# Performance work log

Hardware: AMD Instinct MI355X
Metric: run time of the kernel (lower is better)

Reference implementation:

```python
import jax, jax.numpy as jnp
import numpy as np

N_USERS = 100000
N_ITEMS = 50000
N_NODES = N_USERS + N_ITEMS
EMB_DIM = 128
N_LAYERS = 3
NNZ = 2400000
MASK_PROB = 0.2


def setup_inputs() -> dict:
    key = jax.random.key(0)
    ks = jax.random.split(key, 8)
    user_emb = jax.random.normal(ks[0], (N_USERS, EMB_DIM), dtype=jnp.float32) * 0.1
    item_emb = jax.random.normal(ks[1], (N_ITEMS, EMB_DIM), dtype=jnp.float32) * 0.1
    adj_rows = jax.random.randint(ks[2], (NNZ,), 0, N_NODES, dtype=jnp.int32)
    adj_cols = jax.random.randint(ks[3], (NNZ,), 0, N_NODES, dtype=jnp.int32)
    # stand-in for symmetric-normalized adjacency values
    adj_vals = jax.random.uniform(ks[4], (NNZ,), dtype=jnp.float32) * (1.0 / 16.0)
    # deterministic version of mask_embeddings' random binary mask
    mask = (jax.random.uniform(ks[5], (N_USERS, EMB_DIM)) > MASK_PROB).astype(jnp.float32)
    # Dense(emb_dim, relu) params (Glorot-like scale)
    attr_w = jax.random.normal(ks[6], (EMB_DIM, EMB_DIM), dtype=jnp.float32) * (1.0 / np.sqrt(EMB_DIM))
    attr_b = jnp.zeros((EMB_DIM,), dtype=jnp.float32)
    return {"user_emb": user_emb, "item_emb": item_emb, "adj_rows": adj_rows,
            "adj_cols": adj_cols, "adj_vals": adj_vals, "mask": mask,
            "attr_w": attr_w, "attr_b": attr_b}


def _spmm(rows, cols, vals, x):
    # sparse [N,N] @ dense [N,d] via gather + segment_sum
    return jax.ops.segment_sum(vals[:, None] * x[cols], rows, num_segments=N_NODES)


def reference(user_emb, item_emb, adj_rows, adj_cols, adj_vals, mask, attr_w, attr_b):
    alpha = 1.0 / (N_LAYERS + 1)
    all_emb = jnp.concatenate([user_emb, item_emb], axis=0)  # [N, d]
    combined = alpha * all_emb
    for _ in range(N_LAYERS):
        all_emb = _spmm(adj_rows, adj_cols, adj_vals, all_emb)
        combined = combined + alpha * all_emb
    user_final = combined[:N_USERS]
    item_final = combined[N_USERS:]
    masked_user_emb = user_final * mask
    predicted_attributes = jax.nn.relu(masked_user_emb @ attr_w + attr_b)
    return (user_final, item_final, masked_user_emb, predicted_attributes, mask)
```

## Files before the change

### kernel.cpp

```cpp
#include <hip/hip_runtime.h>

#define N_USERS 100000
#define N_ITEMS 50000
#define N_NODES 150000
#define NNZ     2400000
#define ALPHA   0.25f
#define VSCALE  262144.0f
#define VINV    (1.0f / 262144.0f)

static __device__ __forceinline__ int xcd_swz(int orig, int q, int rem) {
    int xcd = orig & 7, idx = orig >> 3;
    return (xcd < rem ? xcd * (q + 1) : rem * (q + 1) + (xcd - rem) * q) + idx;
}

static __device__ __forceinline__ float wave_max64(float m) {
    #pragma unroll
    for (int off = 32; off >= 1; off >>= 1)
        m = fmaxf(m, __shfl_xor(m, off, 64));
    return m;
}

static __device__ __forceinline__ float i8lo(unsigned short w) {
    return (float)(signed char)(w & 0xff);
}
static __device__ __forceinline__ float i8hi(unsigned short w) {
    return (float)(signed char)(w >> 8);
}

__launch_bounds__(256)
__global__ void k_initq(const float2* __restrict__ ue2, const float2* __restrict__ ie2,
                        unsigned short* __restrict__ xq, float* __restrict__ scl) {
    int r = blockIdx.x * 4 + __builtin_amdgcn_readfirstlane(threadIdx.x >> 6);
    if (r >= N_NODES) return;
    int l = threadIdx.x & 63;
    float2 v = (r < N_USERS) ? ue2[r * 64 + l] : ie2[(r - N_USERS) * 64 + l];
    float m = wave_max64(fmaxf(fabsf(v.x), fabsf(v.y)));
    float inv = (m > 0.f) ? 127.0f / m : 0.f;
    int q0 = (int)rintf(v.x * inv), q1 = (int)rintf(v.y * inv);
    xq[r * 64 + l] = (unsigned short)((q0 & 0xff) | ((q1 & 0xff) << 8));
    if (l == 0) scl[r] = m * (1.0f / 127.0f);
}

__global__ void k_histrank(const int* __restrict__ rows, int* __restrict__ cnt,
                           int* __restrict__ rank) {
    int stride = gridDim.x * blockDim.x;
    for (int i = blockIdx.x * blockDim.x + threadIdx.x; i < NNZ; i += stride)
        rank[i] = atomicAdd(&cnt[rows[i]], 1);
}

__global__ void k_scan1(const int* __restrict__ cnt, int* __restrict__ tmp, int* __restrict__ part) {
    __shared__ int sm[1024];
    int g = blockIdx.x * 1024 + threadIdx.x;
    int v = (g < N_NODES) ? cnt[g] : 0;
    sm[threadIdx.x] = v;
    __syncthreads();
    for (int off = 1; off < 1024; off <<= 1) {
        int t = (threadIdx.x >= off) ? sm[threadIdx.x - off] : 0;
        __syncthreads();
        sm[threadIdx.x] += t;
        __syncthreads();
    }
    if (g < N_NODES) tmp[g] = sm[threadIdx.x];
    if (threadIdx.x == 1023) part[blockIdx.x] = sm[1023];
}

__global__ void k_scan2(int* __restrict__ part, int n) {
    __shared__ int sm[256];
    int v = (threadIdx.x < n) ? part[threadIdx.x] : 0;
    sm[threadIdx.x] = v;
    __syncthreads();
    for (int off = 1; off < 256; off <<= 1) {
        int t = (threadIdx.x >= off) ? sm[threadIdx.x - off] : 0;
        __syncthreads();
        sm[threadIdx.x] += t;
        __syncthreads();
    }
    if (threadIdx.x < n) part[threadIdx.x] = sm[threadIdx.x];
}

__global__ void k_scan3(const int* __restrict__ tmp, const int* __restrict__ part, int* __restrict__ rp) {
    int g = blockIdx.x * 1024 + threadIdx.x;
    if (g < N_NODES) {
        int add = blockIdx.x ? part[blockIdx.x - 1] : 0;
        rp[g + 1] = tmp[g] + add;
    }
    if (g == 0) rp[0] = 0;
}

__launch_bounds__(256)
__global__ void k_scatter(const int* __restrict__ rows, const int* __restrict__ cols,
                          const float* __restrict__ vals, const int* __restrict__ rank,
                          const int* __restrict__ rp, unsigned int* __restrict__ ev) {
    int cls = blockIdx.x & 7;
    int base = (blockIdx.x >> 3) * 256 + threadIdx.x;
    for (int i = base; i < NNZ; i += 65536) {
        int r = rows[i];
        if (((r >> 11) & 7) != cls) continue;
        int v14 = (int)(vals[i] * VSCALE + 0.5f);
        v14 = min(v14, 16383);
        unsigned int w = ((unsigned int)cols[i] << 14) | (unsigned int)v14;
        ev[rp[r] + rank[i]] = w;
    }
}

__launch_bounds__(256)
__global__ void k_spmmq(const int* __restrict__ rp, const unsigned int* __restrict__ ev,
                        const unsigned short* __restrict__ xq, const float* __restrict__ sclx,
                        unsigned short* __restrict__ yq, float* __restrict__ scly) {
    int b = xcd_swz(blockIdx.x, 4687, 4);
    int r = b * 4 + __builtin_amdgcn_readfirstlane(threadIdx.x >> 6);
    if (r >= N_NODES) return;
    int l = threadIdx.x & 63;
    float ax = 0.f, ay = 0.f;
    int s = rp[r], e = rp[r + 1];
    int j = s;
    for (; j + 4 <= e; j += 4) {
        unsigned int m0 = ev[j], m1 = ev[j + 1], m2 = ev[j + 2], m3 = ev[j + 3];
        int c0 = __builtin_amdgcn_readfirstlane((int)(m0 >> 14));
        int c1 = __builtin_amdgcn_readfirstlane((int)(m1 >> 14));
        int c2 = __builtin_amdgcn_readfirstlane((int)(m2 >> 14));
        int c3 = __builtin_amdgcn_readfirstlane((int)(m3 >> 14));
        unsigned short w0 = xq[c0 * 64 + l];
        unsigned short w1 = xq[c1 * 64 + l];
        unsigned short w2 = xq[c2 * 64 + l];
        unsigned short w3 = xq[c3 * 64 + l];
        float f0 = (float)(m0 & 16383u) * VINV * sclx[c0];
        float f1 = (float)(m1 & 16383u) * VINV * sclx[c1];
        float f2 = (float)(m2 & 16383u) * VINV * sclx[c2];
        float f3 = (float)(m3 & 16383u) * VINV * sclx[c3];
        ax += f0 * i8lo(w0) + f1 * i8lo(w1) + f2 * i8lo(w2) + f3 * i8lo(w3);
        ay += f0 * i8hi(w0) + f1 * i8hi(w1) + f2 * i8hi(w2) + f3 * i8hi(w3);
    }
    for (; j < e; ++j) {
        unsigned int m = ev[j];
        int c = __builtin_amdgcn_readfirstlane((int)(m >> 14));
        unsigned short w = xq[c * 64 + l];
        float f = (float)(m & 16383u) * VINV * sclx[c];
        ax += f * i8lo(w);
        ay += f * i8hi(w);
    }
    float m = wave_max64(fmaxf(fabsf(ax), fabsf(ay)));
    float inv = (m > 0.f) ? 127.0f / m : 0.f;
    int q0 = (int)rintf(ax * inv), q1 = (int)rintf(ay * inv);
    yq[r * 64 + l] = (unsigned short)((q0 & 0xff) | ((q1 & 0xff) << 8));
    if (l == 0) scly[r] = m * (1.0f / 127.0f);
}

__launch_bounds__(256)
__global__ void k_spmm3q(const int* __restrict__ rp, const unsigned int* __restrict__ ev,
                         const unsigned short* __restrict__ y2q, const float* __restrict__ scl2,
                         const unsigned short* __restrict__ y1q, const float* __restrict__ scl1,
                         const float2* __restrict__ ue2, const float2* __restrict__ ie2,
                         const float2* __restrict__ mask2,
                         float2* __restrict__ comb2, float2* __restrict__ masked2,
                         float2* __restrict__ maskO2) {
    int b = xcd_swz(blockIdx.x, 4687, 4);
    int r = b * 4 + __builtin_amdgcn_readfirstlane(threadIdx.x >> 6);
    if (r >= N_NODES) return;
    int l = threadIdx.x & 63;
    float ax = 0.f, ay = 0.f;
    int s = rp[r], e = rp[r + 1];
    int j = s;
    for (; j + 4 <= e; j += 4) {
        unsigned int m0 = ev[j], m1 = ev[j + 1], m2 = ev[j + 2], m3 = ev[j + 3];
        int c0 = __builtin_amdgcn_readfirstlane((int)(m0 >> 14));
        int c1 = __builtin_amdgcn_readfirstlane((int)(m1 >> 14));
        int c2 = __builtin_amdgcn_readfirstlane((int)(m2 >> 14));
        int c3 = __builtin_amdgcn_readfirstlane((int)(m3 >> 14));
        unsigned short w0 = y2q[c0 * 64 + l];
        unsigned short w1 = y2q[c1 * 64 + l];
        unsigned short w2 = y2q[c2 * 64 + l];
        unsigned short w3 = y2q[c3 * 64 + l];
        float f0 = (float)(m0 & 16383u) * VINV * scl2[c0];
        float f1 = (float)(m1 & 16383u) * VINV * scl2[c1];
        float f2 = (float)(m2 & 16383u) * VINV * scl2[c2];
        float f3 = (float)(m3 & 16383u) * VINV * scl2[c3];
        ax += f0 * i8lo(w0) + f1 * i8lo(w1) + f2 * i8lo(w2) + f3 * i8lo(w3);
        ay += f0 * i8hi(w0) + f1 * i8hi(w1) + f2 * i8hi(w2) + f3 * i8hi(w3);
    }
    for (; j < e; ++j) {
        unsigned int m = ev[j];
        int c = __builtin_amdgcn_readfirstlane((int)(m >> 14));
        unsigned short w = y2q[c * 64 + l];
        float f = (float)(m & 16383u) * VINV * scl2[c];
        ax += f * i8lo(w);
        ay += f * i8hi(w);
    }
    float2 em = (r < N_USERS) ? ue2[r * 64 + l] : ie2[(r - N_USERS) * 64 + l];
    float s1 = scl1[r], s2 = scl2[r];
    unsigned short a1 = y1q[r * 64 + l];
    unsigned short a2 = y2q[r * 64 + l];
    float cx = ALPHA * (em.x + s1 * i8lo(a1) + s2 * i8lo(a2) + ax);
    float cy = ALPHA * (em.y + s1 * i8hi(a1) + s2 * i8hi(a2) + ay);
    comb2[r * 64 + l] = make_float2(cx, cy);
    if (r < N_USERS) {
        float2 m = mask2[r * 64 + l];
        masked2[r * 64 + l] = make_float2(cx * m.x, cy * m.y);
        maskO2[r * 64 + l]  = m;
    }
}

__launch_bounds__(256)
__global__ void k_mm(const float* __restrict__ A, const float* __restrict__ W,
                     const float* __restrict__ b, float* __restrict__ pred) {
    __shared__ float Wl[128 * 128];
    float4* W4s = (float4*)Wl;
    const float4* W4g = (const float4*)W;
    for (int i = threadIdx.x; i < 4096; i += 256) W4s[i] = W4g[i];
    __syncthreads();

    int rowt = threadIdx.x >> 3;
    int colg = threadIdx.x & 7;
    int row  = blockIdx.x * 32 + rowt;
    const float* ar = A + row * 128;

    float4 a0 = make_float4(0, 0, 0, 0), a1 = a0, a2 = a0, a3 = a0;
    for (int k = 0; k < 128; ++k) {
        float av = ar[k];
        float4 w0 = W4s[k * 32 + colg];
        float4 w1 = W4s[k * 32 + colg + 8];
        float4 w2 = W4s[k * 32 + colg + 16];
        float4 w3 = W4s[k * 32 + colg + 24];
        a0.x += av * w0.x; a0.y += av * w0.y; a0.z += av * w0.z; a0.w += av * w0.w;
        a1.x += av * w1.x; a1.y += av * w1.y; a1.z += av * w1.z; a1.w += av * w1.w;
        a2.x += av * w2.x; a2.y += av * w2.y; a2.z += av * w2.z; a2.w += av * w2.w;
        a3.x += av * w3.x; a3.y += av * w3.y; a3.z += av * w3.z; a3.w += av * w3.w;
    }
    const float4* b4 = (const float4*)b;
    float4* out4 = (float4*)pred;
    float4 acc[4] = {a0, a1, a2, a3};
    #pragma unroll
    for (int jj = 0; jj < 4; ++jj) {
        float4 bb = b4[colg + 8 * jj];
        float4 r;
        r.x = fmaxf(acc[jj].x + bb.x, 0.f);
        r.y = fmaxf(acc[jj].y + bb.y, 0.f);
        r.z = fmaxf(acc[jj].z + bb.z, 0.f);
        r.w = fmaxf(acc[jj].w + bb.w, 0.f);
        out4[row * 32 + colg + 8 * jj] = r;
    }
}

extern "C" void kernel_launch(void* const* d_in, const int* in_sizes, int n_in,
                              void* d_out, int out_size, void* d_ws, size_t ws_size,
                              hipStream_t stream) {
    const float* ue     = (const float*)d_in[0];
    const float* ie     = (const float*)d_in[1];
    const int*   arows  = (const int*)d_in[2];
    const int*   acols  = (const int*)d_in[3];
    const float* avals  = (const float*)d_in[4];
    const float* mask   = (const float*)d_in[5];
    const float* attr_w = (const float*)d_in[6];
    const float* attr_b = (const float*)d_in[7];
    float* out = (float*)d_out;

    float* comb   = out;
    float* masked = out + 19200000;
    float* pred   = out + 32000000;
    float* maskO  = out + 44800000;

    char* ws = (char*)d_ws;
    unsigned short* x0q  = (unsigned short*)(ws);
    unsigned short* y1q  = (unsigned short*)(ws + 19200000);
    unsigned short* y2q  = (unsigned short*)(ws + 38400000);
    float*          scl0 = (float*)        (ws + 57600000);
    float*          scl1 = (float*)        (ws + 58200000);
    float*          scl2 = (float*)        (ws + 58800000);
    int*            rank = (int*)          (ws + 59400000);
    unsigned int*   ev   = (unsigned int*) (ws + 69000000);
    int*            cnt  = (int*)          (ws + 78600000);
    int*            rp   = (int*)          (ws + 79200064);
    int*            tmp  = (int*)          (ws + 79800128);
    int*            part = (int*)          (ws + 80400192);

    hipMemsetAsync(cnt, 0, (N_NODES + 1) * sizeof(int), stream);
    k_initq<<<37500, 256, 0, stream>>>((const float2*)ue, (const float2*)ie, x0q, scl0);
    k_histrank<<<2048, 256, 0, stream>>>(arows, cnt, rank);
    k_scan1<<<147, 1024, 0, stream>>>(cnt, tmp, part);
    k_scan2<<<1, 256, 0, stream>>>(part, 147);
    k_scan3<<<147, 1024, 0, stream>>>(tmp, part, rp);
    k_scatter<<<2048, 256, 0, stream>>>(arows, acols, avals, rank, rp, ev);

    k_spmmq<<<37500, 256, 0, stream>>>(rp, ev, x0q, scl0, y1q, scl1);
    k_spmmq<<<37500, 256, 0, stream>>>(rp, ev, y1q, scl1, y2q, scl2);
    k_spmm3q<<<37500, 256, 0, stream>>>(rp, ev, y2q, scl2, y1q, scl1,
                                        (const float2*)ue, (const float2*)ie,
                                        (const float2*)mask,
                                        (float2*)comb, (float2*)masked, (float2*)maskO);

    k_mm<<<3125, 256, 0, stream>>>(masked, attr_w, attr_b, pred);
}
```

Measured before the change: 878.6 us.

## Process each row with half-waves using 4-byte int8 packed loads and nontemporal stores

Each 32-lane half-wave now handles one node row and each lane loads four int8 features as one 32-bit word, so every wave gathers two rows per edge step. Dropping readfirstlane lets the two halves index different neighbors. The change also uses nontemporal loads and stores for streamed outputs and inputs, and 16-byte vectors in the final fused kernel. This cuts instruction count per gathered byte and widens memory transactions, at the cost of per-lane (non-scalar) column indices and scales, and a scattered access pattern within a wave.

```diff
diff --git a/kernel.cpp b/kernel.cpp
--- a/kernel.cpp
+++ b/kernel.cpp
@@ -8,36 +8,42 @@
 #define VSCALE  262144.0f
 #define VINV    (1.0f / 262144.0f)
 
+typedef float f32x4 __attribute__((ext_vector_type(4)));
+
 static __device__ __forceinline__ int xcd_swz(int orig, int q, int rem) {
     int xcd = orig & 7, idx = orig >> 3;
     return (xcd < rem ? xcd * (q + 1) : rem * (q + 1) + (xcd - rem) * q) + idx;
 }
 
-static __device__ __forceinline__ float wave_max64(float m) {
+static __device__ __forceinline__ f32x4 ntld4(const f32x4* p) { return __builtin_nontemporal_load(p); }
+static __device__ __forceinline__ unsigned int ntldu(const unsigned int* p) { return __builtin_nontemporal_load(p); }
+static __device__ __forceinline__ void ntst4(f32x4* p, f32x4 v) { __builtin_nontemporal_store(v, p); }
+static __device__ __forceinline__ void ntstu(unsigned int* p, unsigned int v) { __builtin_nontemporal_store(v, p); }
+
+static __device__ __forceinline__ float b0(unsigned int w) { return (float)(signed char)(w); }
+static __device__ __forceinline__ float b1(unsigned int w) { return (float)(signed char)(w >> 8); }
+static __device__ __forceinline__ float b2(unsigned int w) { return (float)(signed char)(w >> 16); }
+static __device__ __forceinline__ float b3(unsigned int w) { return (float)(signed char)(w >> 24); }
+
+static __device__ __forceinline__ float half_max32(float m) {
     #pragma unroll
-    for (int off = 32; off >= 1; off >>= 1)
-        m = fmaxf(m, __shfl_xor(m, off, 64));
+    for (int off = 16; off >= 1; off >>= 1)
+        m = fmaxf(m, __shfl_xor(m, off, 32));
     return m;
 }
 
-static __device__ __forceinline__ float i8lo(unsigned short w) {
-    return (float)(signed char)(w & 0xff);
-}
-static __device__ __forceinline__ float i8hi(unsigned short w) {
-    return (float)(signed char)(w >> 8);
-}
-
-__launch_bounds__(256)
-__global__ void k_initq(const float2* __restrict__ ue2, const float2* __restrict__ ie2,
-                        unsigned short* __restrict__ xq, float* __restrict__ scl) {
-    int r = blockIdx.x * 4 + __builtin_amdgcn_readfirstlane(threadIdx.x >> 6);
-    if (r >= N_NODES) return;
-    int l = threadIdx.x & 63;
-    float2 v = (r < N_USERS) ? ue2[r * 64 + l] : ie2[(r - N_USERS) * 64 + l];
-    float m = wave_max64(fmaxf(fabsf(v.x), fabsf(v.y)));
+__launch_bounds__(256)
+__global__ void k_initq(const f32x4* __restrict__ ue4, const f32x4* __restrict__ ie4,
+                        unsigned int* __restrict__ xq32, float* __restrict__ scl) {
+    int r = blockIdx.x * 8 + (threadIdx.x >> 5);
+    int l = threadIdx.x & 31;
+    f32x4 v = (r < N_USERS) ? ue4[r * 32 + l] : ie4[(r - N_USERS) * 32 + l];
+    float m = half_max32(fmaxf(fmaxf(fabsf(v.x), fabsf(v.y)), fmaxf(fabsf(v.z), fabsf(v.w))));
     float inv = (m > 0.f) ? 127.0f / m : 0.f;
     int q0 = (int)rintf(v.x * inv), q1 = (int)rintf(v.y * inv);
-    xq[r * 64 + l] = (unsigned short)((q0 & 0xff) | ((q1 & 0xff) << 8));
+    int q2 = (int)rintf(v.z * inv), q3 = (int)rintf(v.w * inv);
+    unsigned int w = (q0 & 0xff) | ((q1 & 0xff) << 8) | ((q2 & 0xff) << 16) | ((unsigned)(q3 & 0xff) << 24);
+    xq32[r * 32 + l] = w;
     if (l == 0) scl[r] = m * (1.0f / 127.0f);
 }
 
@@ -103,100 +109,101 @@
     }
 }
 
-__launch_bounds__(256)
-__global__ void k_spmmq(const int* __restrict__ rp, const unsigned int* __restrict__ ev,
-                        const unsigned short* __restrict__ xq, const float* __restrict__ sclx,
-                        unsigned short* __restrict__ yq, float* __restrict__ scly) {
-    int b = xcd_swz(blockIdx.x, 4687, 4);
-    int r = b * 4 + __builtin_amdgcn_readfirstlane(threadIdx.x >> 6);
-    if (r >= N_NODES) return;
-    int l = threadIdx.x & 63;
-    float ax = 0.f, ay = 0.f;
+template<int LAYER>
+__launch_bounds__(256)
+__global__ void k_spmm2(const int* __restrict__ rp, const unsigned int* __restrict__ ev,
+                        const unsigned int* __restrict__ xq32, const float* __restrict__ sclx,
+                        unsigned int* __restrict__ yq32, float* __restrict__ scly) {
+    int b = xcd_swz(blockIdx.x, 2343, 6);
+    int r = b * 8 + (threadIdx.x >> 5);
+    int l = threadIdx.x & 31;
+    float a0 = 0.f, a1 = 0.f, a2 = 0.f, a3 = 0.f;
     int s = rp[r], e = rp[r + 1];
     int j = s;
     for (; j + 4 <= e; j += 4) {
         unsigned int m0 = ev[j], m1 = ev[j + 1], m2 = ev[j + 2], m3 = ev[j + 3];
-        int c0 = __builtin_amdgcn_readfirstlane((int)(m0 >> 14));
-        int c1 = __builtin_amdgcn_readfirstlane((int)(m1 >> 14));
-        int c2 = __builtin_amdgcn_readfirstlane((int)(m2 >> 14));
-        int c3 = __builtin_amdgcn_readfirstlane((int)(m3 >> 14));
-        unsigned short w0 = xq[c0 * 64 + l];
-        unsigned short w1 = xq[c1 * 64 + l];
-        unsigned short w2 = xq[c2 * 64 + l];
-        unsigned short w3 = xq[c3 * 64 + l];
+        unsigned int c0 = m0 >> 14, c1 = m1 >> 14, c2 = m2 >> 14, c3 = m3 >> 14;
+        unsigned int w0 = xq32[c0 * 32 + l];
+        unsigned int w1 = xq32[c1 * 32 + l];
+        unsigned int w2 = xq32[c2 * 32 + l];
+        unsigned int w3 = xq32[c3 * 32 + l];
         float f0 = (float)(m0 & 16383u) * VINV * sclx[c0];
         float f1 = (float)(m1 & 16383u) * VINV * sclx[c1];
         float f2 = (float)(m2 & 16383u) * VINV * sclx[c2];
         float f3 = (float)(m3 & 16383u) * VINV * sclx[c3];
-        ax += f0 * i8lo(w0) + f1 * i8lo(w1) + f2 * i8lo(w2) + f3 * i8lo(w3);
-        ay += f0 * i8hi(w0) + f1 * i8hi(w1) + f2 * i8hi(w2) + f3 * i8hi(w3);
+        a0 += f0 * b0(w0) + f1 * b0(w1) + f2 * b0(w2) + f3 * b0(w3);
+        a1 += f0 * b1(w0) + f1 * b1(w1) + f2 * b1(w2) + f3 * b1(w3);
+        a2 += f0 * b2(w0) + f1 * b2(w1) + f2 * b2(w2) + f3 * b2(w3);
+        a3 += f0 * b3(w0) + f1 * b3(w1) + f2 * b3(w2) + f3 * b3(w3);
     }
     for (; j < e; ++j) {
         unsigned int m = ev[j];
-        int c = __builtin_amdgcn_readfirstlane((int)(m >> 14));
-        unsigned short w = xq[c * 64 + l];
+        unsigned int c = m >> 14;
+        unsigned int w = xq32[c * 32 + l];
         float f = (float)(m & 16383u) * VINV * sclx[c];
-        ax += f * i8lo(w);
-        ay += f * i8hi(w);
-    }
-    float m = wave_max64(fmaxf(fabsf(ax), fabsf(ay)));
+        a0 += f * b0(w); a1 += f * b1(w); a2 += f * b2(w); a3 += f * b3(w);
+    }
+    float m = half_max32(fmaxf(fmaxf(fabsf(a0), fabsf(a1)), fmaxf(fabsf(a2), fabsf(a3))));
     float inv = (m > 0.f) ? 127.0f / m : 0.f;
-    int q0 = (int)rintf(ax * inv), q1 = (int)rintf(ay * inv);
-    yq[r * 64 + l] = (unsigned short)((q0 & 0xff) | ((q1 & 0xff) << 8));
+    int q0 = (int)rintf(a0 * inv), q1 = (int)rintf(a1 * inv);
+    int q2 = (int)rintf(a2 * inv), q3 = (int)rintf(a3 * inv);
+    unsigned int w = (q0 & 0xff) | ((q1 & 0xff) << 8) | ((q2 & 0xff) << 16) | ((unsigned)(q3 & 0xff) << 24);
+    ntstu(yq32 + r * 32 + l, w);
     if (l == 0) scly[r] = m * (1.0f / 127.0f);
 }
 
 __launch_bounds__(256)
-__global__ void k_spmm3q(const int* __restrict__ rp, const unsigned int* __restrict__ ev,
-                         const unsigned short* __restrict__ y2q, const float* __restrict__ scl2,
-                         const unsigned short* __restrict__ y1q, const float* __restrict__ scl1,
-                         const float2* __restrict__ ue2, const float2* __restrict__ ie2,
-                         const float2* __restrict__ mask2,
-                         float2* __restrict__ comb2, float2* __restrict__ masked2,
-                         float2* __restrict__ maskO2) {
-    int b = xcd_swz(blockIdx.x, 4687, 4);
-    int r = b * 4 + __builtin_amdgcn_readfirstlane(threadIdx.x >> 6);
-    if (r >= N_NODES) return;
-    int l = threadIdx.x & 63;
-    float ax = 0.f, ay = 0.f;
+__global__ void k_spmm3f(const int* __restrict__ rp, const unsigned int* __restrict__ ev,
+                         const unsigned int* __restrict__ y2q, const float* __restrict__ scl2,
+                         const unsigned int* __restrict__ y1q, const float* __restrict__ scl1,
+                         const f32x4* __restrict__ ue4, const f32x4* __restrict__ ie4,
+                         const f32x4* __restrict__ mask4,
+                         f32x4* __restrict__ comb4, f32x4* __restrict__ masked4,
+                         f32x4* __restrict__ maskO4) {
+    int b = xcd_swz(blockIdx.x, 2343, 6);
+    int r = b * 8 + (threadIdx.x >> 5);
+    int l = threadIdx.x & 31;
+    float a0 = 0.f, a1 = 0.f, a2 = 0.f, a3 = 0.f;
     int s = rp[r], e = rp[r + 1];
     int j = s;
     for (; j + 4 <= e; j += 4) {
         unsigned int m0 = ev[j], m1 = ev[j + 1], m2 = ev[j + 2], m3 = ev[j + 3];
-        int c0 = __builtin_amdgcn_readfirstlane((int)(m0 >> 14));
-        int c1 = __builtin_amdgcn_readfirstlane((int)(m1 >> 14));
-        int c2 = __builtin_amdgcn_readfirstlane((int)(m2 >> 14));
-        int c3 = __builtin_amdgcn_readfirstlane((int)(m3 >> 14));
-        unsigned short w0 = y2q[c0 * 64 + l];
-        unsigned short w1 = y2q[c1 * 64 + l];
-        unsigned short w2 = y2q[c2 * 64 + l];
-        unsigned short w3 = y2q[c3 * 64 + l];
+        unsigned int c0 = m0 >> 14, c1 = m1 >> 14, c2 = m2 >> 14, c3 = m3 >> 14;
+        unsigned int w0 = y2q[c0 * 32 + l];
+        unsigned int w1 = y2q[c1 * 32 + l];
+        unsigned int w2 = y2q[c2 * 32 + l];
+        unsigned int w3 = y2q[c3 * 32 + l];
         float f0 = (float)(m0 & 16383u) * VINV * scl2[c0];
         float f1 = (float)(m1 & 16383u) * VINV * scl2[c1];
         float f2 = (float)(m2 & 16383u) * VINV * scl2[c2];
         float f3 = (float)(m3 & 16383u) * VINV * scl2[c3];
-        ax += f0 * i8lo(w0) + f1 * i8lo(w1) + f2 * i8lo(w2) + f3 * i8lo(w3);
-        ay += f0 * i8hi(w0) + f1 * i8hi(w1) + f2 * i8hi(w2) + f3 * i8hi(w3);
+        a0 += f0 * b0(w0) + f1 * b0(w1) + f2 * b0(w2) + f3 * b0(w3);
+        a1 += f0 * b1(w0) + f1 * b1(w1) + f2 * b1(w2) + f3 * b1(w3);
+        a2 += f0 * b2(w0) + f1 * b2(w1) + f2 * b2(w2) + f3 * b2(w3);
+        a3 += f0 * b3(w0) + f1 * b3(w1) + f2 * b3(w2) + f3 * b3(w3);
     }
     for (; j < e; ++j) {
         unsigned int m = ev[j];
-        int c = __builtin_amdgcn_readfirstlane((int)(m >> 14));
-        unsigned short w = y2q[c * 64 + l];
+        unsigned int c = m >> 14;
+        unsigned int w = y2q[c * 32 + l];
         float f = (float)(m & 16383u) * VINV * scl2[c];
-        ax += f * i8lo(w);
-        ay += f * i8hi(w);
-    }
-    float2 em = (r < N_USERS) ? ue2[r * 64 + l] : ie2[(r - N_USERS) * 64 + l];
+        a0 += f * b0(w); a1 += f * b1(w); a2 += f * b2(w); a3 += f * b3(w);
+    }
+    f32x4 em = (r < N_USERS) ? ntld4(ue4 + r * 32 + l) : ntld4(ie4 + (r - N_USERS) * 32 + l);
     float s1 = scl1[r], s2 = scl2[r];
-    unsigned short a1 = y1q[r * 64 + l];
-    unsigned short a2 = y2q[r * 64 + l];
-    float cx = ALPHA * (em.x + s1 * i8lo(a1) + s2 * i8lo(a2) + ax);
-    float cy = ALPHA * (em.y + s1 * i8hi(a1) + s2 * i8hi(a2) + ay);
-    comb2[r * 64 + l] = make_float2(cx, cy);
+    unsigned int u1 = ntldu(y1q + r * 32 + l);
+    unsigned int u2 = ntldu(y2q + r * 32 + l);
+    f32x4 c;
+    c.x = ALPHA * (em.x + s1 * b0(u1) + s2 * b0(u2) + a0);
+    c.y = ALPHA * (em.y + s1 * b1(u1) + s2 * b1(u2) + a1);
+    c.z = ALPHA * (em.z + s1 * b2(u1) + s2 * b2(u2) + a2);
+    c.w = ALPHA * (em.w + s1 * b3(u1) + s2 * b3(u2) + a3);
+    ntst4(comb4 + r * 32 + l, c);
     if (r < N_USERS) {
-        float2 m = mask2[r * 64 + l];
-        masked2[r * 64 + l] = make_float2(cx * m.x, cy * m.y);
-        maskO2[r * 64 + l]  = m;
+        f32x4 m4 = ntld4(mask4 + r * 32 + l);
+        f32x4 md; md.x = c.x * m4.x; md.y = c.y * m4.y; md.z = c.z * m4.z; md.w = c.w * m4.w;
+        ntst4(masked4 + r * 32 + l, md);
+        ntst4(maskO4 + r * 32 + l, m4);
     }
 }
 
@@ -227,17 +234,17 @@
         a3.x += av * w3.x; a3.y += av * w3.y; a3.z += av * w3.z; a3.w += av * w3.w;
     }
     const float4* b4 = (const float4*)b;
-    float4* out4 = (float4*)pred;
+    f32x4* out4 = (f32x4*)pred;
     float4 acc[4] = {a0, a1, a2, a3};
     #pragma unroll
     for (int jj = 0; jj < 4; ++jj) {
         float4 bb = b4[colg + 8 * jj];
-        float4 r;
-        r.x = fmaxf(acc[jj].x + bb.x, 0.f);
-        r.y = fmaxf(acc[jj].y + bb.y, 0.f);
-        r.z = fmaxf(acc[jj].z + bb.z, 0.f);
-        r.w = fmaxf(acc[jj].w + bb.w, 0.f);
-        out4[row * 32 + colg + 8 * jj] = r;
+        f32x4 rr;
+        rr.x = fmaxf(acc[jj].x + bb.x, 0.f);
+        rr.y = fmaxf(acc[jj].y + bb.y, 0.f);
+        rr.z = fmaxf(acc[jj].z + bb.z, 0.f);
+        rr.w = fmaxf(acc[jj].w + bb.w, 0.f);
+        ntst4(out4 + row * 32 + colg + 8 * jj, rr);
     }
 }
 
@@ -260,33 +267,33 @@
     float* maskO  = out + 44800000;
 
     char* ws = (char*)d_ws;
-    unsigned short* x0q  = (unsigned short*)(ws);
-    unsigned short* y1q  = (unsigned short*)(ws + 19200000);
-    unsigned short* y2q  = (unsigned short*)(ws + 38400000);
-    float*          scl0 = (float*)        (ws + 57600000);
-    float*          scl1 = (float*)        (ws + 58200000);
-    float*          scl2 = (float*)        (ws + 58800000);
-    int*            rank = (int*)          (ws + 59400000);
-    unsigned int*   ev   = (unsigned int*) (ws + 69000000);
-    int*            cnt  = (int*)          (ws + 78600000);
-    int*            rp   = (int*)          (ws + 79200064);
-    int*            tmp  = (int*)          (ws + 79800128);
-    int*            part = (int*)          (ws + 80400192);
+    unsigned int* x0q  = (unsigned int*)(ws);
+    unsigned int* y1q  = (unsigned int*)(ws + 19200000);
+    unsigned int* y2q  = (unsigned int*)(ws + 38400000);
+    float*        scl0 = (float*)       (ws + 57600000);
+    float*        scl1 = (float*)       (ws + 58200000);
+    float*        scl2 = (float*)       (ws + 58800000);
+    int*          rank = (int*)         (ws + 59400000);
+    unsigned int* ev   = (unsigned int*)(ws + 69000000);
+    int*          cnt  = (int*)         (ws + 78600000);
+    int*          rp   = (int*)         (ws + 79200064);
+    int*          tmp  = (int*)         (ws + 79800128);
+    int*          part = (int*)         (ws + 80400192);
 
     hipMemsetAsync(cnt, 0, (N_NODES + 1) * sizeof(int), stream);
-    k_initq<<<37500, 256, 0, stream>>>((const float2*)ue, (const float2*)ie, x0q, scl0);
+    k_initq<<<18750, 256, 0, stream>>>((const f32x4*)ue, (const f32x4*)ie, x0q, scl0);
     k_histrank<<<2048, 256, 0, stream>>>(arows, cnt, rank);
     k_scan1<<<147, 1024, 0, stream>>>(cnt, tmp, part);
     k_scan2<<<1, 256, 0, stream>>>(part, 147);
     k_scan3<<<147, 1024, 0, stream>>>(tmp, part, rp);
     k_scatter<<<2048, 256, 0, stream>>>(arows, acols, avals, rank, rp, ev);
 
-    k_spmmq<<<37500, 256, 0, stream>>>(rp, ev, x0q, scl0, y1q, scl1);
-    k_spmmq<<<37500, 256, 0, stream>>>(rp, ev, y1q, scl1, y2q, scl2);
-    k_spmm3q<<<37500, 256, 0, stream>>>(rp, ev, y2q, scl2, y1q, scl1,
-                                        (const float2*)ue, (const float2*)ie,
-                                        (const float2*)mask,
-                                        (float2*)comb, (float2*)masked, (float2*)maskO);
+    k_spmm2<1><<<18750, 256, 0, stream>>>(rp, ev, x0q, scl0, y1q, scl1);
+    k_spmm2<2><<<18750, 256, 0, stream>>>(rp, ev, y1q, scl1, y2q, scl2);
+    k_spmm3f<<<18750, 256, 0, stream>>>(rp, ev, y2q, scl2, y1q, scl1,
+                                        (const f32x4*)ue, (const f32x4*)ie,
+                                        (const f32x4*)mask,
+                                        (f32x4*)comb, (f32x4*)masked, (f32x4*)maskO);
 
     k_mm<<<3125, 256, 0, stream>>>(masked, attr_w, attr_b, pred);
 }
```

Result: faster. 835.3 us (-4.9%).
